# Optimization experiments

Hardware: AMD Instinct MI355X
Metric: run time of the kernel (lower is better)

## Reference

```python
import jax, jax.numpy as jnp
import numpy as np

B, N = 8, 50000
DIM, C_DIM, TASK_DIM, H, NB, OUT = 3, 64, 512, 64, 5, 12


def setup_inputs() -> dict:
    key = jax.random.key(0)
    ks = jax.random.split(key, 16)
    s = lambda fan_in: 1.0 / np.sqrt(fan_in)
    inp = {
        "p": jax.random.normal(ks[0], (B, N, DIM), dtype=jnp.float32),
        "c": jax.random.normal(ks[1], (B, N, C_DIM), dtype=jnp.float32),
        "task_feature": jax.random.normal(ks[2], (B, TASK_DIM), dtype=jnp.float32),
        # params (stored as [in, out] so y = x @ W + b)
        "fc_p_W": jax.random.uniform(ks[3], (DIM, H), jnp.float32, -s(DIM), s(DIM)),
        "fc_p_b": jax.random.uniform(ks[4], (H,), jnp.float32, -s(DIM), s(DIM)),
        "fc_c_W": jax.random.uniform(ks[5], (NB, C_DIM + TASK_DIM, H), jnp.float32, -s(C_DIM + TASK_DIM), s(C_DIM + TASK_DIM)),
        "fc_c_b": jax.random.uniform(ks[6], (NB, H), jnp.float32, -s(C_DIM + TASK_DIM), s(C_DIM + TASK_DIM)),
        "blk0_W": jax.random.uniform(ks[7], (NB, H, H), jnp.float32, -s(H), s(H)),
        "blk0_b": jax.random.uniform(ks[8], (NB, H), jnp.float32, -s(H), s(H)),
        "blk1_W": jax.random.uniform(ks[9], (NB, H, H), jnp.float32, -s(H), s(H)) * 0.1,
        "blk1_b": jax.random.uniform(ks[10], (NB, H), jnp.float32, -s(H), s(H)),
        "fc_out_W": jax.random.uniform(ks[11], (H, OUT), jnp.float32, -s(H), s(H)),
        "fc_out_b": jax.random.uniform(ks[12], (OUT,), jnp.float32, -s(H), s(H)),
    }
    return inp


def reference(p, c, task_feature, fc_p_W, fc_p_b, fc_c_W, fc_c_b,
              blk0_W, blk0_b, blk1_W, blk1_b, fc_out_W, fc_out_b):
    b, n = p.shape[0], p.shape[1]
    # expand task feature to every point and concat with point-wise code c
    tf = jnp.broadcast_to(task_feature[:, None, :], (b, n, task_feature.shape[-1]))
    cc = jnp.concatenate([c, tf], axis=-1)              # [B, N, 576]
    net = p @ fc_p_W + fc_p_b                           # [B, N, H]
    for i in range(fc_c_W.shape[0]):
        net = net + cc @ fc_c_W[i] + fc_c_b[i]          # conditioning
        # ResnetBlockFC: dx = fc_1(relu(fc_0(relu(x)))); out = x + dx
        h = jax.nn.relu(net) @ blk0_W[i] + blk0_b[i]
        dx = jax.nn.relu(h) @ blk1_W[i] + blk1_b[i]
        net = net + dx
    out = jax.nn.relu(net) @ fc_out_W + fc_out_b        # [B, N, 12]
    return out
```

## Files before the change

kernel.cpp:

```cpp
#include <hip/hip_runtime.h>

#define B_    8
#define N_    50000
#define NB_   5
#define OUT_  12
#define TILES_ 4
#define TILES_PER_BATCH 3125
#define BLOCKS_PER_BATCH 782

typedef _Float16 half8 __attribute__((ext_vector_type(8)));
typedef float   floatx4 __attribute__((ext_vector_type(4)));

__device__ __forceinline__ half8 ldg8(const _Float16* p) {
    union { uint4 u; half8 h; } x;
    x.u = *(const uint4*)p;
    return x.h;
}

__device__ __forceinline__ half8 packB(floatx4 a, floatx4 b) {
    half8 r;
    r[0] = (_Float16)fmaxf(a[0], 0.f); r[1] = (_Float16)fmaxf(a[1], 0.f);
    r[2] = (_Float16)fmaxf(a[2], 0.f); r[3] = (_Float16)fmaxf(a[3], 0.f);
    r[4] = (_Float16)fmaxf(b[0], 0.f); r[5] = (_Float16)fmaxf(b[1], 0.f);
    r[6] = (_Float16)fmaxf(b[2], 0.f); r[7] = (_Float16)fmaxf(b[3], 0.f);
    return r;
}

__device__ __forceinline__ void load8(half8 (&A)[8], const _Float16* base, int q16m) {
    #pragma unroll
    for (int T = 0; T < 4; ++T)
        #pragma unroll
        for (int h = 0; h < 2; ++h)
            A[T * 2 + h] = ldg8(base + (size_t)(T * 128 + h * 64 + q16m) * 8);
}

__global__ void prep_kernel(const float* __restrict__ fc_c_W,
                            const float* __restrict__ blk0_W,
                            const float* __restrict__ blk1_W,
                            const float* __restrict__ fc_out_W,
                            const float* __restrict__ tf,
                            _Float16* __restrict__ ws_w,
                            _Float16* __restrict__ ws_fco,
                            float* __restrict__ partials, int R) {
    int bid = blockIdx.x, tid = threadIdx.x;
    if (bid < 32) {
        int u = bid * 256 + tid;
        if (u < 7680) {
            int m15 = u & 15, q = (u >> 4) & 3, h = (u >> 6) & 1, T = (u >> 7) & 3;
            int mi = u >> 9;
            int mat = mi / 5, i = mi % 5;
            int n = T * 16 + m15;
            _Float16 out[8];
            #pragma unroll
            for (int j = 0; j < 8; ++j) {
                float v;
                if (mat == 0) {
                    int k = 32 * h + 8 * q + j;
                    v = fc_c_W[((size_t)i * 576 + k) * 64 + n];
                } else {
                    int f = 32 * h + 16 * (j >> 2) + 4 * q + (j & 3);
                    const float* W = (mat == 1) ? blk0_W : blk1_W;
                    v = W[((size_t)i * 64 + f) * 64 + n];
                }
                out[j] = (_Float16)v;
            }
            uint4 val = *(uint4*)out;
            for (int r = 0; r < R; ++r)
                *(uint4*)(ws_w + (size_t)r * 61440 + (size_t)u * 8) = val;
        } else {
            int e = u - 7680;
            _Float16 out[8] = {};
            if (e < 128) {
                int m15 = e & 15, q = (e >> 4) & 3, h = (e >> 6) & 1;
                #pragma unroll
                for (int j = 0; j < 8; ++j) {
                    int f = 32 * h + 16 * (j >> 2) + 4 * q + (j & 3);
                    out[j] = (m15 < OUT_) ? (_Float16)fc_out_W[f * OUT_ + m15] : (_Float16)0.f;
                }
            }
            uint4 val = *(uint4*)out;
            for (int r = 0; r < R; ++r)
                *(uint4*)(ws_fco + (size_t)r * 4096 + (size_t)e * 8) = val;
        }
    } else {
        int idx2 = bid - 32;
        int b = idx2 / 10, rem = idx2 % 10, i = rem >> 1, hf = rem & 1;
        int g = tid >> 6, j = tid & 63;
        const float* W  = fc_c_W + ((size_t)i * 576 + 64) * 64;
        const float* tb = tf + b * 512;
        int t0 = hf * 256 + g * 64;
        float acc = 0.f;
        #pragma unroll 8
        for (int t = 0; t < 64; ++t)
            acc += tb[t0 + t] * W[(size_t)(t0 + t) * 64 + j];
        partials[(((b * 5 + i) << 3) + (hf * 4 + g)) * 64 + j] = acc;
    }
}

__global__ void finalize_tp(const float* __restrict__ partials,
                            const float* __restrict__ fc_c_b,
                            const float* __restrict__ fc_p_b,
                            float* __restrict__ tp) {
    int u = blockIdx.x * 256 + threadIdx.x;
    if (u >= 2560) return;
    int b = u / 320, rem = u % 320, i = rem >> 6, j = rem & 63;
    float s = fc_c_b[i * 64 + j] + ((i == 0) ? fc_p_b[j] : 0.f);
    #pragma unroll
    for (int k = 0; k < 8; ++k)
        s += partials[(((b * 5 + i) << 3) + k) * 64 + j];
    tp[u] = s;
}

__device__ __forceinline__ void resblock(
    half8 (&Ac)[8], half8 (&Ab)[8],
    floatx4 (&net4)[TILES_][4], const half8 (&cB)[TILES_][2],
    int tc, int i, int q, int q16m,
    const float* __restrict__ tp_b, const float* __restrict__ b0g,
    const float* __restrict__ b1g, const _Float16* __restrict__ wsr,
    const _Float16* __restrict__ next_cond_base, bool last)
{
    floatx4 tpv[4], bb0[4], bb1[4];
    #pragma unroll
    for (int T = 0; T < 4; ++T) {
        int off = i * 64 + 16 * T + 4 * q;
        tpv[T] = *(const floatx4*)(tp_b + off);
        bb0[T] = *(const floatx4*)(b0g + off);
        bb1[T] = *(const floatx4*)(b1g + off);
    }
    #pragma unroll
    for (int t = 0; t < TILES_; ++t) {
        if (t >= tc) break;
        #pragma unroll
        for (int T = 0; T < 4; ++T) {
            floatx4 a = net4[t][T];
            a = __builtin_amdgcn_mfma_f32_16x16x32_f16(Ac[2 * T], cB[t][0], a, 0, 0, 0);
            a = __builtin_amdgcn_mfma_f32_16x16x32_f16(Ac[2 * T + 1], cB[t][1], a, 0, 0, 0);
            net4[t][T] = a + tpv[T];
        }
    }
    load8(Ac, wsr + (size_t)(10 + i) * 4096, q16m);
    #pragma unroll
    for (int t = 0; t < TILES_; ++t) {
        if (t >= tc) break;
        half8 Bn0 = packB(net4[t][0], net4[t][1]);
        half8 Bn1 = packB(net4[t][2], net4[t][3]);
        floatx4 hh[4];
        #pragma unroll
        for (int T = 0; T < 4; ++T) {
            floatx4 a = bb0[T];
            a = __builtin_amdgcn_mfma_f32_16x16x32_f16(Ab[2 * T], Bn0, a, 0, 0, 0);
            a = __builtin_amdgcn_mfma_f32_16x16x32_f16(Ab[2 * T + 1], Bn1, a, 0, 0, 0);
            hh[T] = a;
        }
        half8 Bh0 = packB(hh[0], hh[1]);
        half8 Bh1 = packB(hh[2], hh[3]);
        #pragma unroll
        for (int T = 0; T < 4; ++T) {
            floatx4 a = bb1[T];
            a = __builtin_amdgcn_mfma_f32_16x16x32_f16(Ac[2 * T], Bh0, a, 0, 0, 0);
            a = __builtin_amdgcn_mfma_f32_16x16x32_f16(Ac[2 * T + 1], Bh1, a, 0, 0, 0);
            net4[t][T] += a;
        }
    }
    load8(Ab, next_cond_base, q16m);
    if (!last)
        load8(Ac, wsr + (size_t)(5 + i + 1) * 4096, q16m);
}

__global__ __launch_bounds__(64, 2) void decoder_kernel(
    const float* __restrict__ p_g, const float* __restrict__ c_g,
    const float* __restrict__ blk0_b, const float* __restrict__ blk1_b,
    const float* __restrict__ fc_p_W, const float* __restrict__ fc_out_b,
    const _Float16* __restrict__ ws_w, const _Float16* __restrict__ ws_fco,
    const float* __restrict__ tp_g, float* __restrict__ out_g, int rmask)
{
    const int bid   = blockIdx.x;
    const int batch = bid / BLOCKS_PER_BATCH;
    const int blk   = bid % BLOCKS_PER_BATCH;
    const int tile0 = blk * TILES_;
    const int tc    = min(TILES_, TILES_PER_BATCH - tile0);
    const long gbase = (long)batch * N_ + (long)tile0 * 16;
    const int lane = threadIdx.x;
    const int q = lane >> 4, m15 = lane & 15;
    const int q16m = q * 16 + m15;
    const _Float16* wsr  = ws_w  + (size_t)(bid & rmask) * 61440;
    const _Float16* fcor = ws_fco + (size_t)(bid & rmask) * 4096;
    const float* tp_b = tp_g + batch * (NB_ * 64);

    half8 X[8], Y[8];
    load8(X, wsr, q16m);
    load8(Y, wsr + (size_t)5 * 4096, q16m);

    half8 cB[TILES_][2];
    #pragma unroll
    for (int t = 0; t < TILES_; ++t) {
        if (t >= tc) break;
        const float* cr = c_g + (size_t)(gbase + t * 16 + m15) * 64;
        #pragma unroll
        for (int h = 0; h < 2; ++h) {
            float4 v0 = *(const float4*)(cr + 32 * h + 8 * q);
            float4 v1 = *(const float4*)(cr + 32 * h + 8 * q + 4);
            half8 r;
            r[0] = (_Float16)v0.x; r[1] = (_Float16)v0.y;
            r[2] = (_Float16)v0.z; r[3] = (_Float16)v0.w;
            r[4] = (_Float16)v1.x; r[5] = (_Float16)v1.y;
            r[6] = (_Float16)v1.z; r[7] = (_Float16)v1.w;
            cB[t][h] = r;
        }
    }

    floatx4 fw[3][4];
    #pragma unroll
    for (int d = 0; d < 3; ++d)
        #pragma unroll
        for (int T = 0; T < 4; ++T)
            fw[d][T] = *(const floatx4*)(fc_p_W + d * 64 + 16 * T + 4 * q);
    floatx4 net4[TILES_][4];
    #pragma unroll
    for (int t = 0; t < TILES_; ++t) {
        if (t >= tc) break;
        long g = gbase + t * 16 + m15;
        float pp0 = p_g[g * 3 + 0], pp1 = p_g[g * 3 + 1], pp2 = p_g[g * 3 + 2];
        #pragma unroll
        for (int T = 0; T < 4; ++T)
            net4[t][T] = fw[0][T] * pp0 + fw[1][T] * pp1 + fw[2][T] * pp2;
    }

    resblock(X, Y, net4, cB, tc, 0, q, q16m, tp_b, blk0_b, blk1_b, wsr, wsr + (size_t)1 * 4096, false);
    resblock(Y, X, net4, cB, tc, 1, q, q16m, tp_b, blk0_b, blk1_b, wsr, wsr + (size_t)2 * 4096, false);
    resblock(X, Y, net4, cB, tc, 2, q, q16m, tp_b, blk0_b, blk1_b, wsr, wsr + (size_t)3 * 4096, false);
    resblock(Y, X, net4, cB, tc, 3, q, q16m, tp_b, blk0_b, blk1_b, wsr, wsr + (size_t)4 * 4096, false);
    resblock(X, Y, net4, cB, tc, 4, q, q16m, tp_b, blk0_b, blk1_b, wsr, fcor, true);

    floatx4 ob = {0.f, 0.f, 0.f, 0.f};
    if (q < 3) ob = *(const floatx4*)(fc_out_b + 4 * q);
    #pragma unroll
    for (int t = 0; t < TILES_; ++t) {
        if (t >= tc) break;
        half8 Bn0 = packB(net4[t][0], net4[t][1]);
        half8 Bn1 = packB(net4[t][2], net4[t][3]);
        floatx4 a = ob;
        a = __builtin_amdgcn_mfma_f32_16x16x32_f16(Y[0], Bn0, a, 0, 0, 0);
        a = __builtin_amdgcn_mfma_f32_16x16x32_f16(Y[1], Bn1, a, 0, 0, 0);
        if (q < 3) {
            long g = gbase + t * 16 + m15;
            *(float4*)(out_g + g * OUT_ + 4 * q) = make_float4(a[0], a[1], a[2], a[3]);
        }
    }
}

extern "C" void kernel_launch(void* const* d_in, const int* in_sizes, int n_in,
                              void* d_out, int out_size, void* d_ws, size_t ws_size,
                              hipStream_t stream) {
    const float* p        = (const float*)d_in[0];
    const float* c        = (const float*)d_in[1];
    const float* tf       = (const float*)d_in[2];
    const float* fc_p_W   = (const float*)d_in[3];
    const float* fc_p_b   = (const float*)d_in[4];
    const float* fc_c_W   = (const float*)d_in[5];
    const float* fc_c_b   = (const float*)d_in[6];
    const float* blk0_W   = (const float*)d_in[7];
    const float* blk0_b   = (const float*)d_in[8];
    const float* blk1_W   = (const float*)d_in[9];
    const float* blk1_b   = (const float*)d_in[10];
    const float* fc_out_W = (const float*)d_in[11];
    const float* fc_out_b = (const float*)d_in[12];
    float* out = (float*)d_out;

    int R = 8;
    while (R > 1 && ((size_t)R * (61440 + 4096) * 2 + 81920 + 10240) > ws_size) R >>= 1;

    _Float16* ws_w   = (_Float16*)d_ws;
    _Float16* ws_fco = ws_w + (size_t)R * 61440;
    float* partials  = (float*)(ws_fco + (size_t)R * 4096);
    float* tp        = partials + 20480;

    prep_kernel<<<112, 256, 0, stream>>>(fc_c_W, blk0_W, blk1_W, fc_out_W, tf,
                                         ws_w, ws_fco, partials, R);
    finalize_tp<<<10, 256, 0, stream>>>(partials, fc_c_b, fc_p_b, tp);
    decoder_kernel<<<B_ * BLOCKS_PER_BATCH, 64, 0, stream>>>(
        p, c, blk0_b, blk1_b, fc_p_W, fc_out_b, ws_w, ws_fco, tp, out, R - 1);
}
```

Baseline: 239.2 us.

## Make decoder persistent and stage all weights into LDS once per block

Replaces the many-small-blocks launch with a persistent grid of 256 blocks of 8 waves. Each block copies all fp16 weights into shared memory once, using asynchronous global-to-LDS loads, and each wave then loops over tile tasks reading weight fragments from LDS instead of global memory. The ReLU in fragment packing also becomes a single vector max on fp16. The aim is to cut repeated global and L2 weight traffic, at the cost of ~125KB of LDS per block, which limits each CU to one block, and of an uneven task split across waves that leaves some waves with an extra task.

```diff
diff --git a/kernel.cpp b/kernel.cpp
--- a/kernel.cpp
+++ b/kernel.cpp
@@ -7,31 +7,37 @@
 #define TILES_ 4
 #define TILES_PER_BATCH 3125
 #define BLOCKS_PER_BATCH 782
+#define NTASKS (B_ * BLOCKS_PER_BATCH)
+#define GRID_  256
+#define NWAVES_TOTAL (GRID_ * 8)
 
 typedef _Float16 half8 __attribute__((ext_vector_type(8)));
 typedef float   floatx4 __attribute__((ext_vector_type(4)));
 
-__device__ __forceinline__ half8 ldg8(const _Float16* p) {
-    union { uint4 u; half8 h; } x;
-    x.u = *(const uint4*)p;
-    return x.h;
+__device__ __forceinline__ void cp16_async(const void* g, void* l) {
+    __builtin_amdgcn_global_load_lds(
+        (const __attribute__((address_space(1))) unsigned int*)g,
+        (__attribute__((address_space(3))) unsigned int*)l,
+        16, 0, 0);
 }
 
 __device__ __forceinline__ half8 packB(floatx4 a, floatx4 b) {
     half8 r;
-    r[0] = (_Float16)fmaxf(a[0], 0.f); r[1] = (_Float16)fmaxf(a[1], 0.f);
-    r[2] = (_Float16)fmaxf(a[2], 0.f); r[3] = (_Float16)fmaxf(a[3], 0.f);
-    r[4] = (_Float16)fmaxf(b[0], 0.f); r[5] = (_Float16)fmaxf(b[1], 0.f);
-    r[6] = (_Float16)fmaxf(b[2], 0.f); r[7] = (_Float16)fmaxf(b[3], 0.f);
-    return r;
-}
-
-__device__ __forceinline__ void load8(half8 (&A)[8], const _Float16* base, int q16m) {
+    r[0] = (_Float16)a[0]; r[1] = (_Float16)a[1];
+    r[2] = (_Float16)a[2]; r[3] = (_Float16)a[3];
+    r[4] = (_Float16)b[0]; r[5] = (_Float16)b[1];
+    r[6] = (_Float16)b[2]; r[7] = (_Float16)b[3];
+    half8 z = {(_Float16)0, (_Float16)0, (_Float16)0, (_Float16)0,
+               (_Float16)0, (_Float16)0, (_Float16)0, (_Float16)0};
+    return __builtin_elementwise_max(r, z);
+}
+
+__device__ __forceinline__ void lds8(half8 (&A)[8], const _Float16* base, int lane) {
     #pragma unroll
     for (int T = 0; T < 4; ++T)
         #pragma unroll
         for (int h = 0; h < 2; ++h)
-            A[T * 2 + h] = ldg8(base + (size_t)(T * 128 + h * 64 + q16m) * 8);
+            A[T * 2 + h] = *(const half8*)(base + (size_t)(T * 128 + h * 64 + lane) * 8);
 }
 
 __global__ void prep_kernel(const float* __restrict__ fc_c_W,
@@ -114,10 +120,10 @@
 __device__ __forceinline__ void resblock(
     half8 (&Ac)[8], half8 (&Ab)[8],
     floatx4 (&net4)[TILES_][4], const half8 (&cB)[TILES_][2],
-    int tc, int i, int q, int q16m,
+    int tc, int i, int q, int lane,
     const float* __restrict__ tp_b, const float* __restrict__ b0g,
-    const float* __restrict__ b1g, const _Float16* __restrict__ wsr,
-    const _Float16* __restrict__ next_cond_base, bool last)
+    const float* __restrict__ b1g, const _Float16* wlds,
+    const _Float16* next_base, bool last)
 {
     floatx4 tpv[4], bb0[4], bb1[4];
     #pragma unroll
@@ -138,7 +144,7 @@
             net4[t][T] = a + tpv[T];
         }
     }
-    load8(Ac, wsr + (size_t)(10 + i) * 4096, q16m);
+    lds8(Ac, wlds + (size_t)(10 + i) * 4096, lane);
     #pragma unroll
     for (int t = 0; t < TILES_; ++t) {
         if (t >= tc) break;
@@ -162,89 +168,109 @@
             net4[t][T] += a;
         }
     }
-    load8(Ab, next_cond_base, q16m);
-    if (!last)
-        load8(Ac, wsr + (size_t)(5 + i + 1) * 4096, q16m);
-}
-
-__global__ __launch_bounds__(64, 2) void decoder_kernel(
+    if (!last) {
+        lds8(Ab, next_base, lane);
+        lds8(Ac, wlds + (size_t)(5 + i + 1) * 4096, lane);
+    } else {
+        Ab[0] = *(const half8*)(next_base + (size_t)lane * 8);
+        Ab[1] = *(const half8*)(next_base + (size_t)(64 + lane) * 8);
+    }
+}
+
+__global__ __launch_bounds__(512, 2) void decoder_kernel(
     const float* __restrict__ p_g, const float* __restrict__ c_g,
     const float* __restrict__ blk0_b, const float* __restrict__ blk1_b,
     const float* __restrict__ fc_p_W, const float* __restrict__ fc_out_b,
     const _Float16* __restrict__ ws_w, const _Float16* __restrict__ ws_fco,
     const float* __restrict__ tp_g, float* __restrict__ out_g, int rmask)
 {
-    const int bid   = blockIdx.x;
-    const int batch = bid / BLOCKS_PER_BATCH;
-    const int blk   = bid % BLOCKS_PER_BATCH;
-    const int tile0 = blk * TILES_;
-    const int tc    = min(TILES_, TILES_PER_BATCH - tile0);
-    const long gbase = (long)batch * N_ + (long)tile0 * 16;
-    const int lane = threadIdx.x;
+    __shared__ __align__(16) _Float16 wlds[62464];
+
+    const int tid  = threadIdx.x;
+    const int wave = tid >> 6;
+    const int lane = tid & 63;
     const int q = lane >> 4, m15 = lane & 15;
-    const int q16m = q * 16 + m15;
-    const _Float16* wsr  = ws_w  + (size_t)(bid & rmask) * 61440;
-    const _Float16* fcor = ws_fco + (size_t)(bid & rmask) * 4096;
-    const float* tp_b = tp_g + batch * (NB_ * 64);
-
-    half8 X[8], Y[8];
-    load8(X, wsr, q16m);
-    load8(Y, wsr + (size_t)5 * 4096, q16m);
-
-    half8 cB[TILES_][2];
-    #pragma unroll
-    for (int t = 0; t < TILES_; ++t) {
-        if (t >= tc) break;
-        const float* cr = c_g + (size_t)(gbase + t * 16 + m15) * 64;
-        #pragma unroll
-        for (int h = 0; h < 2; ++h) {
-            float4 v0 = *(const float4*)(cr + 32 * h + 8 * q);
-            float4 v1 = *(const float4*)(cr + 32 * h + 8 * q + 4);
-            half8 r;
-            r[0] = (_Float16)v0.x; r[1] = (_Float16)v0.y;
-            r[2] = (_Float16)v0.z; r[3] = (_Float16)v0.w;
-            r[4] = (_Float16)v1.x; r[5] = (_Float16)v1.y;
-            r[6] = (_Float16)v1.z; r[7] = (_Float16)v1.w;
-            cB[t][h] = r;
-        }
-    }
-
-    floatx4 fw[3][4];
-    #pragma unroll
-    for (int d = 0; d < 3; ++d)
-        #pragma unroll
-        for (int T = 0; T < 4; ++T)
-            fw[d][T] = *(const floatx4*)(fc_p_W + d * 64 + 16 * T + 4 * q);
-    floatx4 net4[TILES_][4];
-    #pragma unroll
-    for (int t = 0; t < TILES_; ++t) {
-        if (t >= tc) break;
-        long g = gbase + t * 16 + m15;
-        float pp0 = p_g[g * 3 + 0], pp1 = p_g[g * 3 + 1], pp2 = p_g[g * 3 + 2];
-        #pragma unroll
-        for (int T = 0; T < 4; ++T)
-            net4[t][T] = fw[0][T] * pp0 + fw[1][T] * pp1 + fw[2][T] * pp2;
-    }
-
-    resblock(X, Y, net4, cB, tc, 0, q, q16m, tp_b, blk0_b, blk1_b, wsr, wsr + (size_t)1 * 4096, false);
-    resblock(Y, X, net4, cB, tc, 1, q, q16m, tp_b, blk0_b, blk1_b, wsr, wsr + (size_t)2 * 4096, false);
-    resblock(X, Y, net4, cB, tc, 2, q, q16m, tp_b, blk0_b, blk1_b, wsr, wsr + (size_t)3 * 4096, false);
-    resblock(Y, X, net4, cB, tc, 3, q, q16m, tp_b, blk0_b, blk1_b, wsr, wsr + (size_t)4 * 4096, false);
-    resblock(X, Y, net4, cB, tc, 4, q, q16m, tp_b, blk0_b, blk1_b, wsr, fcor, true);
-
-    floatx4 ob = {0.f, 0.f, 0.f, 0.f};
-    if (q < 3) ob = *(const floatx4*)(fc_out_b + 4 * q);
-    #pragma unroll
-    for (int t = 0; t < TILES_; ++t) {
-        if (t >= tc) break;
-        half8 Bn0 = packB(net4[t][0], net4[t][1]);
-        half8 Bn1 = packB(net4[t][2], net4[t][3]);
-        floatx4 a = ob;
-        a = __builtin_amdgcn_mfma_f32_16x16x32_f16(Y[0], Bn0, a, 0, 0, 0);
-        a = __builtin_amdgcn_mfma_f32_16x16x32_f16(Y[1], Bn1, a, 0, 0, 0);
-        if (q < 3) {
+    const _Float16* wsr = ws_w  + (size_t)(blockIdx.x & rmask) * 61440;
+    const _Float16* fcr = ws_fco + (size_t)(blockIdx.x & rmask) * 4096;
+
+    #pragma unroll
+    for (int k = 0; k < 16; ++k) {
+        int cb = k * 512 + wave * 64;
+        if (cb < 7808) {
+            const _Float16* src = (cb < 7680) ? (wsr + (size_t)cb * 8)
+                                              : (fcr + (size_t)(cb - 7680) * 8);
+            cp16_async(src + (size_t)lane * 8, (char*)&wlds[0] + (size_t)cb * 16);
+        }
+    }
+    __syncthreads();
+
+    for (int task = blockIdx.x * 8 + wave; task < NTASKS; task += NWAVES_TOTAL) {
+        const int batch = task / BLOCKS_PER_BATCH;
+        const int blk   = task % BLOCKS_PER_BATCH;
+        const int tile0 = blk * TILES_;
+        const int tc    = min(TILES_, TILES_PER_BATCH - tile0);
+        const long gbase = (long)batch * N_ + (long)tile0 * 16;
+        const float* tp_b = tp_g + batch * (NB_ * 64);
+
+        half8 cB[TILES_][2];
+        #pragma unroll
+        for (int t = 0; t < TILES_; ++t) {
+            if (t >= tc) break;
+            const float* cr = c_g + (size_t)(gbase + t * 16 + m15) * 64;
+            #pragma unroll
+            for (int h = 0; h < 2; ++h) {
+                float4 v0 = *(const float4*)(cr + 32 * h + 8 * q);
+                float4 v1 = *(const float4*)(cr + 32 * h + 8 * q + 4);
+                half8 r;
+                r[0] = (_Float16)v0.x; r[1] = (_Float16)v0.y;
+                r[2] = (_Float16)v0.z; r[3] = (_Float16)v0.w;
+                r[4] = (_Float16)v1.x; r[5] = (_Float16)v1.y;
+                r[6] = (_Float16)v1.z; r[7] = (_Float16)v1.w;
+                cB[t][h] = r;
+            }
+        }
+
+        half8 X[8], Y[8];
+        lds8(X, &wlds[0], lane);
+        lds8(Y, &wlds[0] + (size_t)5 * 4096, lane);
+
+        floatx4 fw[3][4];
+        #pragma unroll
+        for (int d = 0; d < 3; ++d)
+            #pragma unroll
+            for (int T = 0; T < 4; ++T)
+                fw[d][T] = *(const floatx4*)(fc_p_W + d * 64 + 16 * T + 4 * q);
+        floatx4 net4[TILES_][4];
+        #pragma unroll
+        for (int t = 0; t < TILES_; ++t) {
+            if (t >= tc) break;
             long g = gbase + t * 16 + m15;
-            *(float4*)(out_g + g * OUT_ + 4 * q) = make_float4(a[0], a[1], a[2], a[3]);
+            float pp0 = p_g[g * 3 + 0], pp1 = p_g[g * 3 + 1], pp2 = p_g[g * 3 + 2];
+            #pragma unroll
+            for (int T = 0; T < 4; ++T)
+                net4[t][T] = fw[0][T] * pp0 + fw[1][T] * pp1 + fw[2][T] * pp2;
+        }
+
+        resblock(X, Y, net4, cB, tc, 0, q, lane, tp_b, blk0_b, blk1_b, &wlds[0], &wlds[0] + (size_t)1 * 4096, false);
+        resblock(Y, X, net4, cB, tc, 1, q, lane, tp_b, blk0_b, blk1_b, &wlds[0], &wlds[0] + (size_t)2 * 4096, false);
+        resblock(X, Y, net4, cB, tc, 2, q, lane, tp_b, blk0_b, blk1_b, &wlds[0], &wlds[0] + (size_t)3 * 4096, false);
+        resblock(Y, X, net4, cB, tc, 3, q, lane, tp_b, blk0_b, blk1_b, &wlds[0], &wlds[0] + (size_t)4 * 4096, false);
+        resblock(X, Y, net4, cB, tc, 4, q, lane, tp_b, blk0_b, blk1_b, &wlds[0], &wlds[0] + (size_t)61440, true);
+
+        floatx4 ob = {0.f, 0.f, 0.f, 0.f};
+        if (q < 3) ob = *(const floatx4*)(fc_out_b + 4 * q);
+        #pragma unroll
+        for (int t = 0; t < TILES_; ++t) {
+            if (t >= tc) break;
+            half8 Bn0 = packB(net4[t][0], net4[t][1]);
+            half8 Bn1 = packB(net4[t][2], net4[t][3]);
+            floatx4 a = ob;
+            a = __builtin_amdgcn_mfma_f32_16x16x32_f16(Y[0], Bn0, a, 0, 0, 0);
+            a = __builtin_amdgcn_mfma_f32_16x16x32_f16(Y[1], Bn1, a, 0, 0, 0);
+            if (q < 3) {
+                long g = gbase + t * 16 + m15;
+                *(float4*)(out_g + g * OUT_ + 4 * q) = make_float4(a[0], a[1], a[2], a[3]);
+            }
         }
     }
 }
@@ -278,6 +304,6 @@
     prep_kernel<<<112, 256, 0, stream>>>(fc_c_W, blk0_W, blk1_W, fc_out_W, tf,
                                          ws_w, ws_fco, partials, R);
     finalize_tp<<<10, 256, 0, stream>>>(partials, fc_c_b, fc_p_b, tp);
-    decoder_kernel<<<B_ * BLOCKS_PER_BATCH, 64, 0, stream>>>(
+    decoder_kernel<<<GRID_, 512, 0, stream>>>(
         p, c, blk0_b, blk1_b, fc_p_W, fc_out_b, ws_w, ws_fco, tp, out, R - 1);
 }
```

After: 740.6 us. +209.6%, slower.
